# Optimization experiments

Measured on AMD Instinct MI355X. Metric: run time of the kernel, lower is better.

Reference implementation:

```python
import jax, jax.numpy as jnp
import numpy as np

B, L, D = 128, 512, 768   # batch, bert tokens, bert hidden
J = 32                    # clause boundaries -> S = J + 1 segments
S = J + 1
DM, DF = 200, 200         # transformer d_model / ffn dim
EPS = 1e-5


def _ln(x, g, b):
    m = x.mean(-1, keepdims=True)
    v = ((x - m) ** 2).mean(-1, keepdims=True)
    return (x - m) / jnp.sqrt(v + EPS) * g + b


def setup_inputs() -> dict:
    key = jax.random.key(0)
    ks = jax.random.split(key, 12)
    sc = 0.02
    hidden_state = jax.random.normal(ks[0], (B, L, D), jnp.float32)
    # strictly increasing, positive clause boundaries < L (non-empty segments)
    seg = L // S  # stride ~= 15 tokens per clause
    jitter = jax.random.randint(ks[1], (B, J), 0, seg).astype(jnp.int32)
    clause_idx = jnp.arange(1, J + 1, dtype=jnp.int32)[None, :] * seg + jitter
    p = lambda k, shp: sc * jax.random.normal(k, shp, jnp.float32)
    z = lambda n: jnp.zeros((n,), jnp.float32)
    return {
        'hidden_state': hidden_state,
        'clause_idx': clause_idx,
        'fc5_w': p(ks[2], (1, D)), 'fc5_b': z(1),
        'fc1_w': p(ks[3], (DM, D)), 'fc1_b': z(DM),
        'attn_in_w': p(ks[4], (3 * DM, DM)), 'attn_in_b': z(3 * DM),
        'attn_out_w': p(ks[5], (DM, DM)), 'attn_out_b': z(DM),
        'ln1_g': jnp.ones((DM,), jnp.float32), 'ln1_b': z(DM),
        'lin1_w': p(ks[6], (DF, DM)), 'lin1_b': z(DF),
        'lin2_w': p(ks[7], (DM, DF)), 'lin2_b': z(DM),
        'ln2_g': jnp.ones((DM,), jnp.float32), 'ln2_b': z(DM),
        'fc_w': p(ks[8], (2, 2 * DM)), 'fc_b': z(2),
    }


def reference(hidden_state, clause_idx, fc5_w, fc5_b, fc1_w, fc1_b,
              attn_in_w, attn_in_b, attn_out_w, attn_out_b,
              ln1_g, ln1_b, lin1_w, lin1_b, lin2_w, lin2_b,
              ln2_g, ln2_b, fc_w, fc_b):
    # ---- ragged per-segment attention pooling (batched_index_select) ----
    t = jnp.arange(L)
    # segment id of each token: number of boundaries <= t  -> [B, L] in [0, S)
    seg_id = jnp.sum(t[None, None, :] >= clause_idx[:, :, None], axis=1)
    scores = jnp.einsum('bld,d->bl', hidden_state, fc5_w[0]) + fc5_b[0]  # fc5
    mask = seg_id[:, None, :] == jnp.arange(S)[None, :, None]            # [B,S,L]
    logits = jnp.where(mask, scores[:, None, :], -jnp.inf)
    w = jax.nn.softmax(logits, axis=-1)        # per-segment softmax over tokens
    pooled = jnp.einsum('bsl,bld->bsd', w, hidden_state)                 # [B,S,D]

    # ---- fc1 + TransformerEncoderLayer (post-norm, 1 head, relu, no dropout)
    x = pooled @ fc1_w.T + fc1_b                                         # [B,S,DM]
    qkv = x @ attn_in_w.T + attn_in_b
    q, k, v = jnp.split(qkv, 3, axis=-1)
    a = jax.nn.softmax(jnp.einsum('bqd,bkd->bqk', q, k) * (1.0 / np.sqrt(DM).item()), axis=-1)
    att = jnp.einsum('bqk,bkd->bqd', a, v) @ attn_out_w.T + attn_out_b
    x = _ln(x + att, ln1_g, ln1_b)
    ff = jax.nn.relu(x @ lin1_w.T + lin1_b) @ lin2_w.T + lin2_b
    x = _ln(x + ff, ln2_g, ln2_b)

    # ---- cat(first-token broadcast, rest) then classifier fc ----
    h = jnp.concatenate([jnp.broadcast_to(x[:, :1, :], (B, S - 1, DM)), x[:, 1:, :]], axis=-1)
    return h @ fc_w.T + fc_b                                             # [B, S-1, 2]
```

## Files before the change

kernel.cpp:

```cpp
#include <hip/hip_runtime.h>

#define NB 128
#define LL 512
#define DD 768
#define JJ 32
#define SS 33
#define DM 200

typedef __attribute__((ext_vector_type(8))) short bf8_t;
typedef __attribute__((ext_vector_type(4))) float f4_t;

static __device__ __forceinline__ unsigned short f2bf(float f) {
  unsigned u = __float_as_uint(f);
  return (unsigned short)((u + 0x7FFFu + ((u >> 16) & 1u)) >> 16);
}

__global__ __launch_bounds__(256) void pool_kernel(
    const float* __restrict__ hidden, const int* __restrict__ clause,
    const float* __restrict__ fc5w, unsigned short* __restrict__ pooled_bf)
{
  int blk = blockIdx.x;
  int b = blk / SS;
  int s = blk - b * SS;
  int t0 = (s == 0) ? 0 : clause[b * JJ + s - 1];
  int t1 = (s == JJ) ? LL : clause[b * JJ + s];
  int nt = t1 - t0;
  if (nt > 64) nt = 64;
  if (nt < 1) nt = 1;

  __shared__ float wsm[64];
  int tid = threadIdx.x;
  int wave = tid >> 6, lane = tid & 63;

  const float4* w4 = (const float4*)fc5w;
  for (int t = t0 + wave; t < t0 + nt; t += 4) {
    const float4* hp = (const float4*)(hidden + ((long long)b * LL + t) * DD);
    float acc = 0.f;
#pragma unroll
    for (int i = 0; i < 3; ++i) {
      float4 h = hp[lane + 64 * i];
      float4 w = w4[lane + 64 * i];
      acc += h.x * w.x + h.y * w.y + h.z * w.z + h.w * w.w;
    }
#pragma unroll
    for (int off = 32; off; off >>= 1) acc += __shfl_xor(acc, off);
    if (lane == 0) wsm[t - t0] = acc;
  }
  __syncthreads();

  if (wave == 0) {
    float v = (lane < nt) ? wsm[lane] : -__builtin_inff();
    float mx = v;
#pragma unroll
    for (int off = 32; off; off >>= 1) mx = fmaxf(mx, __shfl_xor(mx, off));
    float e = (lane < nt) ? __expf(v - mx) : 0.f;
    float sm = e;
#pragma unroll
    for (int off = 32; off; off >>= 1) sm += __shfl_xor(sm, off);
    if (lane < nt) wsm[lane] = e / sm;
  }
  __syncthreads();

  if (tid < 192) {
    const float4* base = (const float4*)(hidden + ((long long)b * LL + t0) * DD);
    float4 acc = make_float4(0.f, 0.f, 0.f, 0.f);
#pragma unroll 2
    for (int t = 0; t < nt; ++t) {
      float w = wsm[t];
      float4 h = base[t * 192 + tid];
      acc.x = fmaf(w, h.x, acc.x); acc.y = fmaf(w, h.y, acc.y);
      acc.z = fmaf(w, h.z, acc.z); acc.w = fmaf(w, h.w, acc.w);
    }
    ushort4 o;
    o.x = f2bf(acc.x); o.y = f2bf(acc.y); o.z = f2bf(acc.z); o.w = f2bf(acc.w);
    *(ushort4*)(pooled_bf + (long long)blk * DD + tid * 4) = o;
  }
}

__global__ __launch_bounds__(256) void convert_w(
    const float* __restrict__ fc1_w, const float* __restrict__ ain_w,
    const float* __restrict__ aout_w, const float* __restrict__ lin1_w,
    const float* __restrict__ lin2_w,
    unsigned short* __restrict__ fc1_wb, unsigned short* __restrict__ ain_wb,
    unsigned short* __restrict__ aout_wb, unsigned short* __restrict__ lin1_wb,
    unsigned short* __restrict__ lin2_wb)
{
  int t = blockIdx.x * 256 + threadIdx.x;
  if (t < 208 * 768) {
    int n = t / 768, k = t - n * 768;
    fc1_wb[t] = f2bf((n < 200) ? fc1_w[n * 768 + k] : 0.f);
    return;
  }
  t -= 208 * 768;
  if (t < 608 * 224) {
    int n = t / 224, k = t - n * 224;
    ain_wb[t] = f2bf((n < 600 && k < 200) ? ain_w[n * 200 + k] : 0.f);
    return;
  }
  t -= 608 * 224;
  if (t < 208 * 224) {
    int n = t / 224, k = t - n * 224;
    aout_wb[t] = f2bf((n < 200 && k < 200) ? aout_w[n * 200 + k] : 0.f);
    return;
  }
  t -= 208 * 224;
  if (t < 208 * 224) {
    int n = t / 224, k = t - n * 224;
    lin1_wb[t] = f2bf((n < 200 && k < 200) ? lin1_w[n * 200 + k] : 0.f);
    return;
  }
  t -= 208 * 224;
  if (t < 208 * 224) {
    int n = t / 224, k = t - n * 224;
    lin2_wb[t] = f2bf((n < 200 && k < 200) ? lin2_w[n * 200 + k] : 0.f);
  }
}

__global__ __launch_bounds__(256) void mfma_gemm(
    const unsigned short* __restrict__ A, int lda,
    const unsigned short* __restrict__ W, int ldw,
    const float* __restrict__ bias, const float* __restrict__ res,
    float* __restrict__ C, int ldc,
    unsigned short* __restrict__ Cb, int ldcb,
    int N, int K, int relu, int ntiles)
{
  int gw = blockIdx.x * 4 + (threadIdx.x >> 6);
  int lane = threadIdx.x & 63;
  int mt = gw / ntiles, nt = gw - mt * ntiles;
  int m0 = mt * 16, n0 = nt * 16;
  int col = lane & 15, quad = lane >> 4;
  int koff = quad * 8;

  const bf8_t* pa = (const bf8_t*)(A + (long long)(m0 + col) * lda + koff);
  const bf8_t* pw = (const bf8_t*)(W + (long long)(n0 + col) * ldw + koff);

  f4_t acc = {0.f, 0.f, 0.f, 0.f};
  int S = K >> 5;
  bf8_t a = pa[0], w = pw[0];
  for (int s = 1; s < S; ++s) {
    bf8_t a2 = pa[4 * s], w2 = pw[4 * s];
    acc = __builtin_amdgcn_mfma_f32_16x16x32_bf16(a, w, acc, 0, 0, 0);
    a = a2; w = w2;
  }
  acc = __builtin_amdgcn_mfma_f32_16x16x32_bf16(a, w, acc, 0, 0, 0);

  int gn = n0 + col;
  float bv = (bias && gn < N) ? bias[gn] : 0.f;
#pragma unroll
  for (int r = 0; r < 4; ++r) {
    int gm = m0 + quad * 4 + r;
    float v = acc[r] + bv;
    if (res && gn < N) v += res[(long long)gm * ldc + gn];
    if (relu) v = fmaxf(v, 0.f);
    if (C && gn < N) C[(long long)gm * ldc + gn] = v;
    if (Cb) Cb[(long long)gm * ldcb + gn] = f2bf(v);
  }
}

__global__ __launch_bounds__(256) void attn_kernel(
    const float* __restrict__ qkv, float* __restrict__ att_f,
    unsigned short* __restrict__ att_b)
{
  __shared__ float shq[SS][DM];
  __shared__ float shk[SS][DM];
  __shared__ float sc[SS][SS + 1];
  int b = blockIdx.x, tid = threadIdx.x;
  const float* qkvg = qkv + (long long)b * SS * 600;

  for (int u = tid; u < SS * 50; u += 256) {
    int i = u / 50, c = u - i * 50;
    const float4* base = (const float4*)(qkvg + (long long)i * 600);
    ((float4*)&shq[i][0])[c] = base[c];
    ((float4*)&shk[i][0])[c] = base[50 + c];
  }
  __syncthreads();

  for (int g = tid; g < SS * 9; g += 256) {
    int i = g / 9, jg = g - i * 9;
    int j0 = jg * 4;
    int jj[4];
#pragma unroll
    for (int t = 0; t < 4; ++t) jj[t] = (j0 + t < SS) ? j0 + t : SS - 1;
    float s0 = 0.f, s1 = 0.f, s2 = 0.f, s3 = 0.f;
    for (int k = 0; k < DM; k += 4) {
      float4 qv = *(const float4*)&shq[i][k];
      float4 k0v = *(const float4*)&shk[jj[0]][k];
      float4 k1v = *(const float4*)&shk[jj[1]][k];
      float4 k2v = *(const float4*)&shk[jj[2]][k];
      float4 k3v = *(const float4*)&shk[jj[3]][k];
      s0 += qv.x * k0v.x + qv.y * k0v.y + qv.z * k0v.z + qv.w * k0v.w;
      s1 += qv.x * k1v.x + qv.y * k1v.y + qv.z * k1v.z + qv.w * k1v.w;
      s2 += qv.x * k2v.x + qv.y * k2v.y + qv.z * k2v.z + qv.w * k2v.w;
      s3 += qv.x * k3v.x + qv.y * k3v.y + qv.z * k3v.z + qv.w * k3v.w;
    }
    const float scale = 0.07071067811865475f;
    float sv[4] = {s0, s1, s2, s3};
#pragma unroll
    for (int t = 0; t < 4; ++t)
      if (j0 + t < SS) sc[i][j0 + t] = sv[t] * scale;
  }
  __syncthreads();

  if (tid < SS) {
    float mx = -__builtin_inff();
    for (int j = 0; j < SS; ++j) mx = fmaxf(mx, sc[tid][j]);
    float sm = 0.f;
    for (int j = 0; j < SS; ++j) { float e = __expf(sc[tid][j] - mx); sc[tid][j] = e; sm += e; }
    float inv = 1.f / sm;
    for (int j = 0; j < SS; ++j) sc[tid][j] *= inv;
  }
  __syncthreads();

  for (int u = tid; u < SS * 50; u += 256) {
    int i = u / 50, d4 = u - i * 50;
    float4 acc = make_float4(0.f, 0.f, 0.f, 0.f);
#pragma unroll 3
    for (int j = 0; j < SS; ++j) {
      float w = sc[i][j];
      float4 v = *(const float4*)(qkvg + (long long)j * 600 + 400 + d4 * 4);
      acc.x = fmaf(w, v.x, acc.x); acc.y = fmaf(w, v.y, acc.y);
      acc.z = fmaf(w, v.z, acc.z); acc.w = fmaf(w, v.w, acc.w);
    }
    long long row = (long long)b * SS + i;
    *(float4*)(att_f + row * DM + d4 * 4) = acc;
    ushort4 o;
    o.x = f2bf(acc.x); o.y = f2bf(acc.y); o.z = f2bf(acc.z); o.w = f2bf(acc.w);
    *(ushort4*)(att_b + row * 224 + d4 * 4) = o;
  }
}

__global__ __launch_bounds__(256) void ln_kernel(
    float* __restrict__ x, const float* __restrict__ g,
    const float* __restrict__ bb, unsigned short* __restrict__ ob, int nrows)
{
  int row = blockIdx.x * 4 + (threadIdx.x >> 6);
  int lane = threadIdx.x & 63;
  if (row >= nrows) return;
  float* p = x + (long long)row * DM;
  float vals[4];
  float s = 0.f;
#pragma unroll
  for (int i = 0; i < 4; ++i) {
    int k = lane + 64 * i;
    vals[i] = (k < DM) ? p[k] : 0.f;
    s += vals[i];
  }
#pragma unroll
  for (int off = 32; off; off >>= 1) s += __shfl_xor(s, off);
  float mean = s * (1.f / DM);
  float vs = 0.f;
#pragma unroll
  for (int i = 0; i < 4; ++i) {
    int k = lane + 64 * i;
    if (k < DM) { float d = vals[i] - mean; vs += d * d; }
  }
#pragma unroll
  for (int off = 32; off; off >>= 1) vs += __shfl_xor(vs, off);
  float rstd = rsqrtf(vs * (1.f / DM) + 1e-5f);
#pragma unroll
  for (int i = 0; i < 4; ++i) {
    int k = lane + 64 * i;
    if (k < DM) {
      float o = (vals[i] - mean) * rstd * g[k] + bb[k];
      p[k] = o;
      if (ob) ob[(long long)row * 224 + k] = f2bf(o);
    }
  }
}

__global__ __launch_bounds__(256) void cls_kernel(
    const float* __restrict__ x, const float* __restrict__ fcw,
    const float* __restrict__ fcb, float* __restrict__ out)
{
  int gw = blockIdx.x * 4 + (threadIdx.x >> 6);
  int lane = threadIdx.x & 63;
  int b = gw >> 5, j = gw & 31;
  const float* x0 = x + (long long)(b * SS) * DM;
  const float* xj = x0 + (long long)(1 + j) * DM;
  float a0 = 0.f, a1 = 0.f;
  for (int k = lane; k < DM; k += 64) {
    float u = x0[k], w = xj[k];
    a0 += u * fcw[k]       + w * fcw[200 + k];
    a1 += u * fcw[400 + k] + w * fcw[600 + k];
  }
#pragma unroll
  for (int off = 32; off; off >>= 1) {
    a0 += __shfl_xor(a0, off);
    a1 += __shfl_xor(a1, off);
  }
  if (lane == 0) {
    out[gw * 2 + 0] = a0 + fcb[0];
    out[gw * 2 + 1] = a1 + fcb[1];
  }
}

extern "C" void kernel_launch(void* const* d_in, const int* in_sizes, int n_in,
                              void* d_out, int out_size, void* d_ws, size_t ws_size,
                              hipStream_t stream)
{
  (void)in_sizes; (void)n_in; (void)out_size; (void)ws_size;
  const float* hidden = (const float*)d_in[0];
  const int*   clause = (const int*)d_in[1];
  const float* fc5_w  = (const float*)d_in[2];
  const float* fc1_w  = (const float*)d_in[4];
  const float* fc1_b  = (const float*)d_in[5];
  const float* ain_w  = (const float*)d_in[6];
  const float* ain_b  = (const float*)d_in[7];
  const float* aout_w = (const float*)d_in[8];
  const float* aout_b = (const float*)d_in[9];
  const float* ln1_g  = (const float*)d_in[10];
  const float* ln1_b  = (const float*)d_in[11];
  const float* lin1_w = (const float*)d_in[12];
  const float* lin1_b = (const float*)d_in[13];
  const float* lin2_w = (const float*)d_in[14];
  const float* lin2_b = (const float*)d_in[15];
  const float* ln2_g  = (const float*)d_in[16];
  const float* ln2_b  = (const float*)d_in[17];
  const float* fc_w   = (const float*)d_in[18];
  const float* fc_b   = (const float*)d_in[19];
  float* out = (float*)d_out;

  const long long R = (long long)NB * SS;
  char* w8 = (char*)d_ws;
  unsigned short* pooled_bf = (unsigned short*)(w8 + 0);
  float*          att_f32   = (float*)(w8 + 0);
  unsigned short* att_bf    = (unsigned short*)(w8 + 3379200);
  float*          x_f32     = (float*)(w8 + 6488064);
  unsigned short* x_bf      = (unsigned short*)(w8 + 9867264);
  unsigned short* y_bf      = x_bf;
  float*          qkv_f32   = (float*)(w8 + 11759616);
  float*          y_f32     = (float*)(w8 + 11759616);
  unsigned short* f1_bf     = (unsigned short*)(w8 + 15138816);
  float*          y2_f32    = (float*)(w8 + 17031168);
  unsigned short* fc1_wb  = (unsigned short*)(w8 + 21897216);
  unsigned short* ain_wb  = (unsigned short*)(w8 + 22216704);
  unsigned short* aout_wb = (unsigned short*)(w8 + 22489088);
  unsigned short* lin1_wb = (unsigned short*)(w8 + 22582272);
  unsigned short* lin2_wb = (unsigned short*)(w8 + 22675456);

  hipMemsetAsync(x_bf, 0, R * 224 * 2, stream);
  convert_w<<<dim3(1702), 256, 0, stream>>>(fc1_w, ain_w, aout_w, lin1_w, lin2_w,
      fc1_wb, ain_wb, aout_wb, lin1_wb, lin2_wb);
  pool_kernel<<<dim3(NB * SS), 256, 0, stream>>>(hidden, clause, fc5_w, pooled_bf);
  mfma_gemm<<<dim3(858), 256, 0, stream>>>(pooled_bf, DD, fc1_wb, DD, fc1_b,
      nullptr, x_f32, DM, x_bf, 224, DM, DD, 0, 13);
  hipMemsetAsync(att_bf, 0, R * 224 * 2, stream);
  mfma_gemm<<<dim3(2508), 256, 0, stream>>>(x_bf, 224, ain_wb, 224, ain_b,
      nullptr, qkv_f32, 600, nullptr, 0, 600, 224, 0, 38);
  attn_kernel<<<dim3(NB), 256, 0, stream>>>(qkv_f32, att_f32, att_bf);
  hipMemsetAsync(f1_bf, 0, R * 224 * 2, stream);
  mfma_gemm<<<dim3(858), 256, 0, stream>>>(att_bf, 224, aout_wb, 224, aout_b,
      x_f32, y_f32, DM, nullptr, 0, DM, 224, 0, 13);
  ln_kernel<<<dim3(1056), 256, 0, stream>>>(y_f32, ln1_g, ln1_b, y_bf, (int)R);
  mfma_gemm<<<dim3(858), 256, 0, stream>>>(y_bf, 224, lin1_wb, 224, lin1_b,
      nullptr, nullptr, DM, f1_bf, 224, DM, 224, 1, 13);
  mfma_gemm<<<dim3(858), 256, 0, stream>>>(f1_bf, 224, lin2_wb, 224, lin2_b,
      y_f32, y2_f32, DM, nullptr, 0, DM, 224, 0, 13);
  ln_kernel<<<dim3(1056), 256, 0, stream>>>(y2_f32, ln2_g, ln2_b, nullptr, (int)R);
  cls_kernel<<<dim3(1024), 256, 0, stream>>>(y2_f32, fc_w, fc_b, out);
}
```

Measured before the change: 429.0 us.

## Fuse post-pooling transformer layer into one per-batch mega kernel

Replaces the chain of GEMM, attention, layernorm and classifier launches (plus memsets) with a single kernel where one 512-thread block processes one batch element end to end, using per-block global scratch and shared memory. Attention scores and P·V now use MFMA instead of scalar FP32 loops, with V stored transposed in bf16. This removes many launches and inter-kernel global round trips, but runs only 128 blocks, so device utilization is low and work is serialized by block-level barriers. It also raises the pool loop unroll factor and drops the padding memsets in favour of in-kernel zeroing.

```diff
diff --git a/kernel.cpp b/kernel.cpp
--- a/kernel.cpp
+++ b/kernel.cpp
@@ -13,6 +13,24 @@
 static __device__ __forceinline__ unsigned short f2bf(float f) {
   unsigned u = __float_as_uint(f);
   return (unsigned short)((u + 0x7FFFu + ((u >> 16) & 1u)) >> 16);
+}
+
+template<int KS>
+static __device__ __forceinline__ f4_t mfma_tile(
+    const unsigned short* pa, const unsigned short* pw)
+{
+  f4_t acc = {0.f, 0.f, 0.f, 0.f};
+  bf8_t a = *(const bf8_t*)pa;
+  bf8_t w = *(const bf8_t*)pw;
+#pragma unroll
+  for (int s = 1; s < KS; ++s) {
+    bf8_t a2 = *(const bf8_t*)(pa + 32 * s);
+    bf8_t w2 = *(const bf8_t*)(pw + 32 * s);
+    acc = __builtin_amdgcn_mfma_f32_16x16x32_bf16(a, w, acc, 0, 0, 0);
+    a = a2; w = w2;
+  }
+  acc = __builtin_amdgcn_mfma_f32_16x16x32_bf16(a, w, acc, 0, 0, 0);
+  return acc;
 }
 
 __global__ __launch_bounds__(256) void pool_kernel(
@@ -64,7 +82,7 @@
   if (tid < 192) {
     const float4* base = (const float4*)(hidden + ((long long)b * LL + t0) * DD);
     float4 acc = make_float4(0.f, 0.f, 0.f, 0.f);
-#pragma unroll 2
+#pragma unroll 4
     for (int t = 0; t < nt; ++t) {
       float w = wsm[t];
       float4 h = base[t * 192 + tid];
@@ -116,181 +134,263 @@
   }
 }
 
-__global__ __launch_bounds__(256) void mfma_gemm(
-    const unsigned short* __restrict__ A, int lda,
-    const unsigned short* __restrict__ W, int ldw,
-    const float* __restrict__ bias, const float* __restrict__ res,
-    float* __restrict__ C, int ldc,
-    unsigned short* __restrict__ Cb, int ldcb,
-    int N, int K, int relu, int ntiles)
+#define SB_XF   0
+#define SB_XB   39936
+#define SB_QB   61440
+#define SB_KB   82944
+#define SB_VT   104448
+#define SB_AB   131072
+#define SB_YF   152576
+#define SB_YB   192512
+#define SB_F1   214016
+#define SB_BLK  235520
+
+__global__ __launch_bounds__(512) void mega_kernel(
+    const unsigned short* __restrict__ pooled,
+    const unsigned short* __restrict__ fc1_wb, const float* __restrict__ fc1_b,
+    const unsigned short* __restrict__ ain_wb, const float* __restrict__ ain_b,
+    const unsigned short* __restrict__ aout_wb, const float* __restrict__ aout_b,
+    const unsigned short* __restrict__ lin1_wb, const float* __restrict__ lin1_b,
+    const unsigned short* __restrict__ lin2_wb, const float* __restrict__ lin2_b,
+    const float* __restrict__ ln1_g, const float* __restrict__ ln1_b,
+    const float* __restrict__ ln2_g, const float* __restrict__ ln2_b,
+    const float* __restrict__ fc_w, const float* __restrict__ fc_b,
+    char* __restrict__ scratch, float* __restrict__ out)
 {
-  int gw = blockIdx.x * 4 + (threadIdx.x >> 6);
-  int lane = threadIdx.x & 63;
-  int mt = gw / ntiles, nt = gw - mt * ntiles;
-  int m0 = mt * 16, n0 = nt * 16;
-  int col = lane & 15, quad = lane >> 4;
-  int koff = quad * 8;
-
-  const bf8_t* pa = (const bf8_t*)(A + (long long)(m0 + col) * lda + koff);
-  const bf8_t* pw = (const bf8_t*)(W + (long long)(n0 + col) * ldw + koff);
-
-  f4_t acc = {0.f, 0.f, 0.f, 0.f};
-  int S = K >> 5;
-  bf8_t a = pa[0], w = pw[0];
-  for (int s = 1; s < S; ++s) {
-    bf8_t a2 = pa[4 * s], w2 = pw[4 * s];
-    acc = __builtin_amdgcn_mfma_f32_16x16x32_bf16(a, w, acc, 0, 0, 0);
-    a = a2; w = w2;
-  }
-  acc = __builtin_amdgcn_mfma_f32_16x16x32_bf16(a, w, acc, 0, 0, 0);
-
-  int gn = n0 + col;
-  float bv = (bias && gn < N) ? bias[gn] : 0.f;
-#pragma unroll
-  for (int r = 0; r < 4; ++r) {
-    int gm = m0 + quad * 4 + r;
-    float v = acc[r] + bv;
-    if (res && gn < N) v += res[(long long)gm * ldc + gn];
-    if (relu) v = fmaxf(v, 0.f);
-    if (C && gn < N) C[(long long)gm * ldc + gn] = v;
-    if (Cb) Cb[(long long)gm * ldcb + gn] = f2bf(v);
-  }
-}
-
-__global__ __launch_bounds__(256) void attn_kernel(
-    const float* __restrict__ qkv, float* __restrict__ att_f,
-    unsigned short* __restrict__ att_b)
-{
-  __shared__ float shq[SS][DM];
-  __shared__ float shk[SS][DM];
-  __shared__ float sc[SS][SS + 1];
-  int b = blockIdx.x, tid = threadIdx.x;
-  const float* qkvg = qkv + (long long)b * SS * 600;
-
-  for (int u = tid; u < SS * 50; u += 256) {
-    int i = u / 50, c = u - i * 50;
-    const float4* base = (const float4*)(qkvg + (long long)i * 600);
-    ((float4*)&shq[i][0])[c] = base[c];
-    ((float4*)&shk[i][0])[c] = base[50 + c];
-  }
-  __syncthreads();
-
-  for (int g = tid; g < SS * 9; g += 256) {
-    int i = g / 9, jg = g - i * 9;
-    int j0 = jg * 4;
-    int jj[4];
-#pragma unroll
-    for (int t = 0; t < 4; ++t) jj[t] = (j0 + t < SS) ? j0 + t : SS - 1;
-    float s0 = 0.f, s1 = 0.f, s2 = 0.f, s3 = 0.f;
-    for (int k = 0; k < DM; k += 4) {
-      float4 qv = *(const float4*)&shq[i][k];
-      float4 k0v = *(const float4*)&shk[jj[0]][k];
-      float4 k1v = *(const float4*)&shk[jj[1]][k];
-      float4 k2v = *(const float4*)&shk[jj[2]][k];
-      float4 k3v = *(const float4*)&shk[jj[3]][k];
-      s0 += qv.x * k0v.x + qv.y * k0v.y + qv.z * k0v.z + qv.w * k0v.w;
-      s1 += qv.x * k1v.x + qv.y * k1v.y + qv.z * k1v.z + qv.w * k1v.w;
-      s2 += qv.x * k2v.x + qv.y * k2v.y + qv.z * k2v.z + qv.w * k2v.w;
-      s3 += qv.x * k3v.x + qv.y * k3v.y + qv.z * k3v.z + qv.w * k3v.w;
-    }
-    const float scale = 0.07071067811865475f;
-    float sv[4] = {s0, s1, s2, s3};
-#pragma unroll
-    for (int t = 0; t < 4; ++t)
-      if (j0 + t < SS) sc[i][j0 + t] = sv[t] * scale;
+  const int b = blockIdx.x, tid = threadIdx.x;
+  const int wv = tid >> 6, lane = tid & 63;
+  const int col = lane & 15, quad = lane >> 4;
+  const int koff = quad * 8;
+
+  char* sb = scratch + (size_t)b * SB_BLK;
+  float*          x_f32  = (float*)(sb + SB_XF);
+  unsigned short* x_bf   = (unsigned short*)(sb + SB_XB);
+  unsigned short* q_bf   = (unsigned short*)(sb + SB_QB);
+  unsigned short* k_bf   = (unsigned short*)(sb + SB_KB);
+  unsigned short* vt_bf  = (unsigned short*)(sb + SB_VT);
+  unsigned short* att_bf = (unsigned short*)(sb + SB_AB);
+  float*          y_f32  = (float*)(sb + SB_YF);
+  unsigned short* y_bf   = (unsigned short*)(sb + SB_YB);
+  unsigned short* f1_bf  = (unsigned short*)(sb + SB_F1);
+
+  __shared__ __align__(16) char smem[27456];
+  float*          sc = (float*)smem;
+  unsigned short* Pb = (unsigned short*)(smem + 9984);
+  float*          y2 = (float*)smem;
+
+  {
+    unsigned short* bufs[6] = {x_bf, q_bf, k_bf, att_bf, y_bf, f1_bf};
+    const uint4 z4 = make_uint4(0, 0, 0, 0);
+    for (int u = tid; u < 6 * 48 * 4; u += 512) {
+      int bi = u / (48 * 4), rem = u - bi * (48 * 4);
+      int row = rem >> 2, c = rem & 3;
+      *(uint4*)(bufs[bi] + row * 224 + 192 + c * 8) = z4;
+    }
+    for (int u = tid; u < 208 * 4; u += 512) {
+      int row = u >> 2, c = u & 3;
+      *(uint4*)(vt_bf + row * 64 + 32 + c * 8) = z4;
+    }
+  }
+  __syncthreads();
+
+  {
+    const unsigned short* Ab = pooled + (size_t)b * SS * DD;
+    for (int t = wv; t < 3 * 13; t += 8) {
+      int mt = t / 13, nt = t - mt * 13;
+      int m0 = mt * 16, n0 = nt * 16;
+      f4_t acc = mfma_tile<24>(Ab + (size_t)(m0 + col) * DD + koff,
+                               fc1_wb + (size_t)(n0 + col) * DD + koff);
+      int gn = n0 + col;
+      if (gn < DM) {
+        float bv = fc1_b[gn];
+#pragma unroll
+        for (int r = 0; r < 4; ++r) {
+          int gm = m0 + quad * 4 + r;
+          float v = acc[r] + bv;
+          x_f32[gm * 208 + gn] = v;
+          x_bf[gm * 224 + gn] = f2bf(v);
+        }
+      }
+    }
+  }
+  __syncthreads();
+
+  for (int t = wv; t < 3 * 38; t += 8) {
+    int mt = t / 38, nt = t - mt * 38;
+    int m0 = mt * 16, n0 = nt * 16;
+    f4_t acc = mfma_tile<7>(x_bf + (m0 + col) * 224 + koff,
+                            ain_wb + (size_t)(n0 + col) * 224 + koff);
+    int gn = n0 + col;
+    if (gn < 600) {
+      float bv = ain_b[gn];
+#pragma unroll
+      for (int r = 0; r < 4; ++r) {
+        int gm = m0 + quad * 4 + r;
+        unsigned short bfv = f2bf(acc[r] + bv);
+        if (gn < 200)      q_bf[gm * 224 + gn] = bfv;
+        else if (gn < 400) k_bf[gm * 224 + (gn - 200)] = bfv;
+        else if (gm < SS)  vt_bf[(gn - 400) * 64 + gm] = bfv;
+      }
+    }
+  }
+  __syncthreads();
+
+  for (int t = wv; t < 9; t += 8) {
+    int mt = t / 3, nt = t - mt * 3;
+    int m0 = mt * 16, n0 = nt * 16;
+    f4_t acc = mfma_tile<7>(q_bf + (m0 + col) * 224 + koff,
+                            k_bf + (n0 + col) * 224 + koff);
+    int gn = n0 + col;
+#pragma unroll
+    for (int r = 0; r < 4; ++r)
+      sc[(m0 + quad * 4 + r) * 52 + gn] = acc[r] * 0.07071067811865475f;
   }
   __syncthreads();
 
   if (tid < SS) {
-    float mx = -__builtin_inff();
-    for (int j = 0; j < SS; ++j) mx = fmaxf(mx, sc[tid][j]);
+    float mx = -1e30f;
+    for (int j = 0; j < SS; ++j) mx = fmaxf(mx, sc[tid * 52 + j]);
     float sm = 0.f;
-    for (int j = 0; j < SS; ++j) { float e = __expf(sc[tid][j] - mx); sc[tid][j] = e; sm += e; }
+    for (int j = 0; j < SS; ++j) { float e = __expf(sc[tid * 52 + j] - mx); sc[tid * 52 + j] = e; sm += e; }
     float inv = 1.f / sm;
-    for (int j = 0; j < SS; ++j) sc[tid][j] *= inv;
-  }
-  __syncthreads();
-
-  for (int u = tid; u < SS * 50; u += 256) {
-    int i = u / 50, d4 = u - i * 50;
-    float4 acc = make_float4(0.f, 0.f, 0.f, 0.f);
-#pragma unroll 3
-    for (int j = 0; j < SS; ++j) {
-      float w = sc[i][j];
-      float4 v = *(const float4*)(qkvg + (long long)j * 600 + 400 + d4 * 4);
-      acc.x = fmaf(w, v.x, acc.x); acc.y = fmaf(w, v.y, acc.y);
-      acc.z = fmaf(w, v.z, acc.z); acc.w = fmaf(w, v.w, acc.w);
-    }
-    long long row = (long long)b * SS + i;
-    *(float4*)(att_f + row * DM + d4 * 4) = acc;
-    ushort4 o;
-    o.x = f2bf(acc.x); o.y = f2bf(acc.y); o.z = f2bf(acc.z); o.w = f2bf(acc.w);
-    *(ushort4*)(att_b + row * 224 + d4 * 4) = o;
-  }
-}
-
-__global__ __launch_bounds__(256) void ln_kernel(
-    float* __restrict__ x, const float* __restrict__ g,
-    const float* __restrict__ bb, unsigned short* __restrict__ ob, int nrows)
-{
-  int row = blockIdx.x * 4 + (threadIdx.x >> 6);
-  int lane = threadIdx.x & 63;
-  if (row >= nrows) return;
-  float* p = x + (long long)row * DM;
-  float vals[4];
-  float s = 0.f;
-#pragma unroll
-  for (int i = 0; i < 4; ++i) {
-    int k = lane + 64 * i;
-    vals[i] = (k < DM) ? p[k] : 0.f;
-    s += vals[i];
-  }
-#pragma unroll
-  for (int off = 32; off; off >>= 1) s += __shfl_xor(s, off);
-  float mean = s * (1.f / DM);
-  float vs = 0.f;
-#pragma unroll
-  for (int i = 0; i < 4; ++i) {
-    int k = lane + 64 * i;
-    if (k < DM) { float d = vals[i] - mean; vs += d * d; }
-  }
-#pragma unroll
-  for (int off = 32; off; off >>= 1) vs += __shfl_xor(vs, off);
-  float rstd = rsqrtf(vs * (1.f / DM) + 1e-5f);
-#pragma unroll
-  for (int i = 0; i < 4; ++i) {
-    int k = lane + 64 * i;
-    if (k < DM) {
-      float o = (vals[i] - mean) * rstd * g[k] + bb[k];
-      p[k] = o;
-      if (ob) ob[(long long)row * 224 + k] = f2bf(o);
-    }
-  }
-}
-
-__global__ __launch_bounds__(256) void cls_kernel(
-    const float* __restrict__ x, const float* __restrict__ fcw,
-    const float* __restrict__ fcb, float* __restrict__ out)
-{
-  int gw = blockIdx.x * 4 + (threadIdx.x >> 6);
-  int lane = threadIdx.x & 63;
-  int b = gw >> 5, j = gw & 31;
-  const float* x0 = x + (long long)(b * SS) * DM;
-  const float* xj = x0 + (long long)(1 + j) * DM;
-  float a0 = 0.f, a1 = 0.f;
-  for (int k = lane; k < DM; k += 64) {
-    float u = x0[k], w = xj[k];
-    a0 += u * fcw[k]       + w * fcw[200 + k];
-    a1 += u * fcw[400 + k] + w * fcw[600 + k];
-  }
-#pragma unroll
-  for (int off = 32; off; off >>= 1) {
-    a0 += __shfl_xor(a0, off);
-    a1 += __shfl_xor(a1, off);
-  }
-  if (lane == 0) {
-    out[gw * 2 + 0] = a0 + fcb[0];
-    out[gw * 2 + 1] = a1 + fcb[1];
+    for (int j = 0; j < SS; ++j) sc[tid * 52 + j] *= inv;
+  }
+  __syncthreads();
+  for (int u = tid; u < 48 * 64; u += 512) {
+    int m = u >> 6, k = u & 63;
+    Pb[m * 72 + k] = (m < SS && k < SS) ? f2bf(sc[m * 52 + k]) : (unsigned short)0;
+  }
+  __syncthreads();
+
+  for (int t = wv; t < 3 * 13; t += 8) {
+    int mt = t / 13, nt = t - mt * 13;
+    int m0 = mt * 16, n0 = nt * 16;
+    f4_t acc = mfma_tile<2>((const unsigned short*)(Pb + (m0 + col) * 72 + koff),
+                            vt_bf + (n0 + col) * 64 + koff);
+    int gn = n0 + col;
+    if (gn < DM) {
+#pragma unroll
+      for (int r = 0; r < 4; ++r)
+        att_bf[(m0 + quad * 4 + r) * 224 + gn] = f2bf(acc[r]);
+    }
+  }
+  __syncthreads();
+
+  for (int t = wv; t < 3 * 13; t += 8) {
+    int mt = t / 13, nt = t - mt * 13;
+    int m0 = mt * 16, n0 = nt * 16;
+    f4_t acc = mfma_tile<7>(att_bf + (m0 + col) * 224 + koff,
+                            aout_wb + (size_t)(n0 + col) * 224 + koff);
+    int gn = n0 + col;
+    if (gn < DM) {
+      float bv = aout_b[gn];
+#pragma unroll
+      for (int r = 0; r < 4; ++r) {
+        int gm = m0 + quad * 4 + r;
+        y_f32[gm * 208 + gn] = acc[r] + bv + x_f32[gm * 208 + gn];
+      }
+    }
+  }
+  __syncthreads();
+
+  for (int r = wv; r < SS; r += 8) {
+    float* p = y_f32 + r * 208;
+    float vals[4]; float s = 0.f;
+#pragma unroll
+    for (int i = 0; i < 4; ++i) { int k = lane + 64 * i; vals[i] = (k < DM) ? p[k] : 0.f; s += vals[i]; }
+#pragma unroll
+    for (int off = 32; off; off >>= 1) s += __shfl_xor(s, off);
+    float mean = s * (1.f / DM);
+    float vs = 0.f;
+#pragma unroll
+    for (int i = 0; i < 4; ++i) { int k = lane + 64 * i; if (k < DM) { float d = vals[i] - mean; vs += d * d; } }
+#pragma unroll
+    for (int off = 32; off; off >>= 1) vs += __shfl_xor(vs, off);
+    float rstd = rsqrtf(vs * (1.f / DM) + 1e-5f);
+#pragma unroll
+    for (int i = 0; i < 4; ++i) {
+      int k = lane + 64 * i;
+      if (k < DM) {
+        float o = (vals[i] - mean) * rstd * ln1_g[k] + ln1_b[k];
+        p[k] = o;
+        y_bf[r * 224 + k] = f2bf(o);
+      }
+    }
+  }
+  __syncthreads();
+
+  for (int t = wv; t < 3 * 13; t += 8) {
+    int mt = t / 13, nt = t - mt * 13;
+    int m0 = mt * 16, n0 = nt * 16;
+    f4_t acc = mfma_tile<7>(y_bf + (m0 + col) * 224 + koff,
+                            lin1_wb + (size_t)(n0 + col) * 224 + koff);
+    int gn = n0 + col;
+    if (gn < DM) {
+      float bv = lin1_b[gn];
+#pragma unroll
+      for (int r = 0; r < 4; ++r)
+        f1_bf[(m0 + quad * 4 + r) * 224 + gn] = f2bf(fmaxf(acc[r] + bv, 0.f));
+    }
+  }
+  __syncthreads();
+
+  for (int t = wv; t < 3 * 13; t += 8) {
+    int mt = t / 13, nt = t - mt * 13;
+    int m0 = mt * 16, n0 = nt * 16;
+    f4_t acc = mfma_tile<7>(f1_bf + (m0 + col) * 224 + koff,
+                            lin2_wb + (size_t)(n0 + col) * 224 + koff);
+    int gn = n0 + col;
+    if (gn < DM) {
+      float bv = lin2_b[gn];
+#pragma unroll
+      for (int r = 0; r < 4; ++r) {
+        int gm = m0 + quad * 4 + r;
+        if (gm < SS) y2[gm * 208 + gn] = acc[r] + bv + y_f32[gm * 208 + gn];
+      }
+    }
+  }
+  __syncthreads();
+
+  for (int r = wv; r < SS; r += 8) {
+    float* p = y2 + r * 208;
+    float vals[4]; float s = 0.f;
+#pragma unroll
+    for (int i = 0; i < 4; ++i) { int k = lane + 64 * i; vals[i] = (k < DM) ? p[k] : 0.f; s += vals[i]; }
+#pragma unroll
+    for (int off = 32; off; off >>= 1) s += __shfl_xor(s, off);
+    float mean = s * (1.f / DM);
+    float vs = 0.f;
+#pragma unroll
+    for (int i = 0; i < 4; ++i) { int k = lane + 64 * i; if (k < DM) { float d = vals[i] - mean; vs += d * d; } }
+#pragma unroll
+    for (int off = 32; off; off >>= 1) vs += __shfl_xor(vs, off);
+    float rstd = rsqrtf(vs * (1.f / DM) + 1e-5f);
+#pragma unroll
+    for (int i = 0; i < 4; ++i) {
+      int k = lane + 64 * i;
+      if (k < DM) p[k] = (vals[i] - mean) * rstd * ln2_g[k] + ln2_b[k];
+    }
+  }
+  __syncthreads();
+
+  for (int j = wv; j < JJ; j += 8) {
+    const float* r0 = y2;
+    const float* rj = y2 + (1 + j) * 208;
+    float a0 = 0.f, a1 = 0.f;
+    for (int k = lane; k < DM; k += 64) {
+      float u = r0[k], w = rj[k];
+      a0 += u * fc_w[k]       + w * fc_w[200 + k];
+      a1 += u * fc_w[400 + k] + w * fc_w[600 + k];
+    }
+#pragma unroll
+    for (int off = 32; off; off >>= 1) {
+      a0 += __shfl_xor(a0, off);
+      a1 += __shfl_xor(a1, off);
+    }
+    if (lane == 0) {
+      out[(b * JJ + j) * 2 + 0] = a0 + fc_b[0];
+      out[(b * JJ + j) * 2 + 1] = a1 + fc_b[1];
+    }
   }
 }
 
@@ -320,42 +420,22 @@
   const float* fc_b   = (const float*)d_in[19];
   float* out = (float*)d_out;
 
-  const long long R = (long long)NB * SS;
   char* w8 = (char*)d_ws;
   unsigned short* pooled_bf = (unsigned short*)(w8 + 0);
-  float*          att_f32   = (float*)(w8 + 0);
-  unsigned short* att_bf    = (unsigned short*)(w8 + 3379200);
-  float*          x_f32     = (float*)(w8 + 6488064);
-  unsigned short* x_bf      = (unsigned short*)(w8 + 9867264);
-  unsigned short* y_bf      = x_bf;
-  float*          qkv_f32   = (float*)(w8 + 11759616);
-  float*          y_f32     = (float*)(w8 + 11759616);
-  unsigned short* f1_bf     = (unsigned short*)(w8 + 15138816);
-  float*          y2_f32    = (float*)(w8 + 17031168);
-  unsigned short* fc1_wb  = (unsigned short*)(w8 + 21897216);
-  unsigned short* ain_wb  = (unsigned short*)(w8 + 22216704);
-  unsigned short* aout_wb = (unsigned short*)(w8 + 22489088);
-  unsigned short* lin1_wb = (unsigned short*)(w8 + 22582272);
-  unsigned short* lin2_wb = (unsigned short*)(w8 + 22675456);
-
-  hipMemsetAsync(x_bf, 0, R * 224 * 2, stream);
+  char* scratch = w8 + 6520832;
+  size_t wbase = 6520832 + (size_t)NB * SB_BLK;
+  unsigned short* fc1_wb  = (unsigned short*)(w8 + wbase);
+  unsigned short* ain_wb  = (unsigned short*)(w8 + wbase + 319488);
+  unsigned short* aout_wb = (unsigned short*)(w8 + wbase + 591872);
+  unsigned short* lin1_wb = (unsigned short*)(w8 + wbase + 685056);
+  unsigned short* lin2_wb = (unsigned short*)(w8 + wbase + 778240);
+
+  pool_kernel<<<dim3(NB * SS), 256, 0, stream>>>(hidden, clause, fc5_w, pooled_bf);
   convert_w<<<dim3(1702), 256, 0, stream>>>(fc1_w, ain_w, aout_w, lin1_w, lin2_w,
       fc1_wb, ain_wb, aout_wb, lin1_wb, lin2_wb);
-  pool_kernel<<<dim3(NB * SS), 256, 0, stream>>>(hidden, clause, fc5_w, pooled_bf);
-  mfma_gemm<<<dim3(858), 256, 0, stream>>>(pooled_bf, DD, fc1_wb, DD, fc1_b,
-      nullptr, x_f32, DM, x_bf, 224, DM, DD, 0, 13);
-  hipMemsetAsync(att_bf, 0, R * 224 * 2, stream);
-  mfma_gemm<<<dim3(2508), 256, 0, stream>>>(x_bf, 224, ain_wb, 224, ain_b,
-      nullptr, qkv_f32, 600, nullptr, 0, 600, 224, 0, 38);
-  attn_kernel<<<dim3(NB), 256, 0, stream>>>(qkv_f32, att_f32, att_bf);
-  hipMemsetAsync(f1_bf, 0, R * 224 * 2, stream);
-  mfma_gemm<<<dim3(858), 256, 0, stream>>>(att_bf, 224, aout_wb, 224, aout_b,
-      x_f32, y_f32, DM, nullptr, 0, DM, 224, 0, 13);
-  ln_kernel<<<dim3(1056), 256, 0, stream>>>(y_f32, ln1_g, ln1_b, y_bf, (int)R);
-  mfma_gemm<<<dim3(858), 256, 0, stream>>>(y_bf, 224, lin1_wb, 224, lin1_b,
-      nullptr, nullptr, DM, f1_bf, 224, DM, 224, 1, 13);
-  mfma_gemm<<<dim3(858), 256, 0, stream>>>(f1_bf, 224, lin2_wb, 224, lin2_b,
-      y_f32, y2_f32, DM, nullptr, 0, DM, 224, 0, 13);
-  ln_kernel<<<dim3(1056), 256, 0, stream>>>(y2_f32, ln2_g, ln2_b, nullptr, (int)R);
-  cls_kernel<<<dim3(1024), 256, 0, stream>>>(y2_f32, fc_w, fc_b, out);
-}
+  mega_kernel<<<dim3(NB), 512, 0, stream>>>(pooled_bf,
+      fc1_wb, fc1_b, ain_wb, ain_b, aout_wb, aout_b,
+      lin1_wb, lin1_b, lin2_wb, lin2_b,
+      ln1_g, ln1_b, ln2_g, ln2_b, fc_w, fc_b,
+      scratch, out);
+}
```

Result: slower. 460.8 us (+7.4%).
